# Optimization experiments

Measured on AMD Instinct MI355X. Metric: run time of the kernel, lower is better.

The kernel has to match this reference:

```python
import jax, jax.numpy as jnp
import numpy as np
import itertools

EPS = 1e-3  # BatchNorm1d eps in the original module
N_VOX = 100000


def _build_sparse_structure():
    """Build realistic clustered voxel coords, a 3x3x3 submanifold neighbor
    table (spconv rulebook equivalent), and the unique-merge mapping used by
    sum_duplicates. All index structure is constant (non-differentiable)."""
    rng = np.random.default_rng(0)
    B, Z, Y, X = 2, 40, 1600, 1408  # sparse_shape = grid_size[::-1] + [1,0,0]
    offs01 = np.array(list(itertools.product([0, 1], repeat=3)), dtype=np.int64)
    coords = []
    for b in range(B):
        base = np.stack([rng.integers(0, Z - 1, 13000),
                         rng.integers(0, Y - 1, 13000),
                         rng.integers(0, X - 1, 13000)], 1)
        exp = (base[:, None, :] + offs01[None]).reshape(-1, 3)  # clustered voxels
        coords.append(np.concatenate([np.full((len(exp), 1), b, np.int64), exp], 1))
    coords = np.unique(np.concatenate(coords, 0), axis=0)[:N_VOX]
    assert len(coords) == N_VOX
    # lexicographic unique order => encoded keys are sorted ascending
    key = ((coords[:, 0] * Z + coords[:, 1]) * Y + coords[:, 2]) * X + coords[:, 3]
    offs27 = np.array(list(itertools.product([-1, 0, 1], repeat=3)), np.int64)
    nc = coords[:, None, 1:] + offs27[None]  # [N,27,3]
    inb = (nc >= 0).all(-1) & (nc[..., 0] < Z) & (nc[..., 1] < Y) & (nc[..., 2] < X)
    nk = ((coords[:, None, 0] * Z + nc[..., 0]) * Y + nc[..., 1]) * X + nc[..., 2]
    pos = np.searchsorted(key, nk).clip(0, N_VOX - 1)
    valid = inb & (key[pos] == nk)
    nbr_idx = np.where(valid, pos, -1).astype(np.int32)  # [N,27], -1 = empty
    # second sparse tensor: half its voxels coincide, half are shifted in x
    coords2 = coords.copy()
    coords2[::2, 3] = np.minimum(coords2[::2, 3] + 1, X - 1)
    comb = np.concatenate([coords, coords2], 0)
    uniq, inv = np.unique(comb, axis=0, return_inverse=True)
    return nbr_idx, inv.astype(np.int32), int(len(uniq))


def setup_inputs() -> dict:
    nbr_idx, seg_ids, num_segments = _build_sparse_structure()
    key = jax.random.key(0)
    ks = jax.random.split(key, 6)
    C = 16
    return {
        'voxel_features': jax.random.normal(ks[0], (N_VOX, C), jnp.float32),
        'feat2': jax.random.normal(ks[1], (N_VOX, C), jnp.float32),
        'W0': jax.random.normal(ks[2], (27, C, 16), jnp.float32) * 0.1,
        'g0': jnp.ones((16,), jnp.float32),
        'b0': jnp.zeros((16,), jnp.float32),
        'W1': jax.random.normal(ks[3], (27, 16, 16), jnp.float32) * 0.1,
        'g1': jnp.ones((16,), jnp.float32),
        'b1': jnp.zeros((16,), jnp.float32),
        'Wobo': jax.random.normal(ks[4], (16, 16), jnp.float32) * 0.1,
        'bobo': jnp.zeros((16,), jnp.float32),
        'Wf': jax.random.normal(ks[5], (16, 128), jnp.float32) * 0.1,
        'bf': jnp.zeros((128,), jnp.float32),
        'nbr_idx': jnp.asarray(nbr_idx),
        'seg_ids': jnp.asarray(seg_ids),
        'num_segments': num_segments,
    }


def _subm_bn_relu(x, W, g, b, nbr_idx):
    """Submanifold 3x3x3 sparse conv (gather->GEMM) + BatchNorm1d + ReLU."""
    N = x.shape[0]
    xp = jnp.concatenate([x, jnp.zeros((1, x.shape[1]), x.dtype)], 0)  # pad row
    idx = jnp.where(nbr_idx < 0, N, nbr_idx)  # missing neighbor -> zero row
    y = jnp.einsum('nkc,kco->no', xp[idx], W)  # [N,27,Cin] x [27,Cin,Cout]
    mu = y.mean(0)
    var = y.var(0)
    return jax.nn.relu((y - mu) * jax.lax.rsqrt(var + EPS) * g + b)


def reference(voxel_features, feat2, W0, g0, b0, W1, g1, b1, Wobo, bobo, Wf, bf,
              nbr_idx, seg_ids, num_segments):
    # level-0 conv_input + conv1 (subm conv, BN, ReLU)
    h = _subm_bn_relu(voxel_features, W0, g0, b0, nbr_idx)
    h = _subm_bn_relu(h, W1, g1, b1, nbr_idx)
    # obo_* 1x1 sparse conv on the second branch (plain matmul + bias)
    t2 = feat2 @ Wobo + bobo
    # sum_duplicates: merge coincident sparse indices by summing features
    comb = jnp.concatenate([h, t2], 0)  # [2N,16]
    merged = jax.ops.segment_sum(comb, seg_ids, num_segments=num_segments)
    # final 1x1 sparse conv
    return merged @ Wf + bf  # [U,128]
```

## Files before the change

### kernel.cpp

```cpp
#include <hip/hip_runtime.h>

#define BN_EPS 1e-3f

using bfrag  = __attribute__((ext_vector_type(8))) short;
using f32x4v = __attribute__((ext_vector_type(4))) float;

__device__ __forceinline__ unsigned short f2bf(float f) {
    union { float f; unsigned u; } v; v.f = f;
    unsigned r = v.u + 0x7FFFu + ((v.u >> 16) & 1u);
    return (unsigned short)(r >> 16);
}

__global__ __launch_bounds__(256)
void prep_kernel(const float* __restrict__ vf,
                 const float* __restrict__ W0, const float* __restrict__ W1,
                 const float* __restrict__ Wf, const int* __restrict__ seg,
                 unsigned short* __restrict__ xb0,
                 unsigned short* __restrict__ Wb0, unsigned short* __restrict__ Wb1,
                 unsigned short* __restrict__ Wfb,
                 float* __restrict__ stats,
                 int* __restrict__ hidx, int* __restrict__ t2s, int N)
{
    int t = blockIdx.x * 256 + threadIdx.x;
    int TA = 2 * (N + 1);
    unsigned short tmp[8];
    if (t < TA) {
        int n = t >> 1, h = t & 1;
        if (n < N) {
            const float* yr = vf + (size_t)n * 16 + h * 8;
#pragma unroll
            for (int j = 0; j < 8; ++j) tmp[j] = f2bf(yr[j]);
        } else {
#pragma unroll
            for (int j = 0; j < 8; ++j) tmp[j] = 0;
        }
        *(int4*)(xb0 + (size_t)n * 16 + h * 8) = *(int4*)tmp;
        return;
    }
    t -= TA;
    if (t < 2 * 14 * 64) {
        int w = t >= 896;
        int l = t - w * 896;
        int s = l >> 6, lane = l & 63;
        int q = lane >> 4, n = lane & 15;
        int tap = 2 * s + (q >> 1);
        int cb  = (q & 1) * 8;
        const float* W = w ? W1 : W0;
        unsigned short* Wb = w ? Wb1 : Wb0;
#pragma unroll
        for (int j = 0; j < 8; ++j)
            tmp[j] = (tap < 27) ? f2bf(W[((size_t)(tap * 16 + cb + j)) * 16 + n]) : 0;
        *(int4*)(Wb + (size_t)l * 8) = *(int4*)tmp;
        return;
    }
    t -= 2 * 14 * 64;
    if (t < 512) {
        int ct = t >> 6, lane = t & 63;
        int q = lane >> 4, n = lane & 15;
#pragma unroll
        for (int j = 0; j < 8; ++j)
            tmp[j] = (q < 2) ? f2bf(Wf[(size_t)(q * 8 + j) * 128 + ct * 16 + n]) : 0;
        *(int4*)(Wfb + (size_t)t * 8) = *(int4*)tmp;
        return;
    }
    t -= 512;
    if (t < 64) { stats[t] = 0.f; return; }
    t -= 64;
    if (t < N) { hidx[seg[t]] = t; return; }
    t -= N;
    if (t < N) {
        int s = seg[N + t];
        if (t == 0 || seg[N + t - 1] != s) t2s[s] = t;
    }
}

__global__ __launch_bounds__(256)
void conv_mfma_kernel(const unsigned short* __restrict__ xb,
                      const unsigned short* __restrict__ Wb,
                      const int* __restrict__ nbr,
                      float* __restrict__ y,
                      float* __restrict__ partials,
                      int N)
{
    __shared__ int   sNbr[64 * 27];
    __shared__ float sred[32];
    int tid = threadIdx.x;
    if (tid < 32) sred[tid] = 0.f;

    int gb = blockIdx.x * 1728;
    int NT = N * 27;
#pragma unroll
    for (int i = 0; i < 7; ++i) {
        int t = i * 256 + tid;
        if (t < 1728) {
            int g = gb + t;
            sNbr[t] = (g < NT) ? nbr[g] : -1;
        }
    }
    __syncthreads();

    int lane = tid & 63, wib = tid >> 6;
    int q = lane >> 4, m = lane & 15;
    int c0   = (q & 1) * 8;
    int tpar = q >> 1;
    int lvox = wib * 16 + m;
    int base = blockIdx.x * 64 + wib * 16;

    int idx[14];
#pragma unroll
    for (int s = 0; s < 14; ++s) {
        int tap = 2 * s + tpar;
        int id  = (tap < 27) ? sNbr[lvox * 27 + tap] : -1;
        idx[s]  = (id >= 0) ? id : N;
    }

    f32x4v acc = {0.f, 0.f, 0.f, 0.f};
#pragma unroll
    for (int s = 0; s < 14; ++s) {
        bfrag a = *(const bfrag*)(xb + (size_t)idx[s] * 16 + c0);
        bfrag b = *(const bfrag*)(Wb + ((size_t)s * 64 + lane) * 8);
        acc = __builtin_amdgcn_mfma_f32_16x16x32_bf16(a, b, acc, 0, 0, 0);
    }

    int o = lane & 15;
#pragma unroll
    for (int i = 0; i < 4; ++i) {
        int row = base + q * 4 + i;
        if (row < N) y[(size_t)row * 16 + o] = acc[i];
    }
    float s  = acc[0] + acc[1] + acc[2] + acc[3];
    float qq = acc[0] * acc[0] + acc[1] * acc[1] + acc[2] * acc[2] + acc[3] * acc[3];
    s  += __shfl_xor(s, 16);  s  += __shfl_xor(s, 32);
    qq += __shfl_xor(qq, 16); qq += __shfl_xor(qq, 32);
    if (lane < 16) {
        atomicAdd(&sred[lane], s);
        atomicAdd(&sred[16 + lane], qq);
    }
    __syncthreads();
    if (tid < 32) partials[(size_t)blockIdx.x * 32 + tid] = sred[tid];
}

__global__ __launch_bounds__(256)
void stats_reduce_kernel(const float* __restrict__ partials,
                         float* __restrict__ stats, int nb)
{
    __shared__ float red[8][32];
    int c = threadIdx.x & 31, sl = threadIdx.x >> 5;
    float s = 0.f;
    for (int i = blockIdx.x * 8 + sl; i < nb; i += gridDim.x * 8)
        s += partials[(size_t)i * 32 + c];
    red[sl][c] = s;
    __syncthreads();
    if (threadIdx.x < 32) {
        float v = 0.f;
#pragma unroll
        for (int k = 0; k < 8; ++k) v += red[k][threadIdx.x];
        atomicAdd(&stats[threadIdx.x], v);
    }
}

__global__ __launch_bounds__(256)
void bnrelu_cvt_kernel(const float* __restrict__ y0, const float* __restrict__ stats,
                       const float* __restrict__ g, const float* __restrict__ b,
                       float invN, unsigned short* __restrict__ xb, int N)
{
    int t = blockIdx.x * 256 + threadIdx.x;
    if (t >= (N + 1) * 2) return;
    int n = t >> 1, h = t & 1;
    unsigned short tmp[8];
    if (n < N) {
        const float* yr = y0 + (size_t)n * 16 + h * 8;
#pragma unroll
        for (int j = 0; j < 8; ++j) {
            int c = h * 8 + j;
            float mu  = stats[c] * invN;
            float var = stats[16 + c] * invN - mu * mu;
            float sc  = g[c] * rsqrtf(var + BN_EPS);
            float v   = fmaxf(fmaf(yr[j], sc, b[c] - mu * sc), 0.f);
            tmp[j] = f2bf(v);
        }
    } else {
#pragma unroll
        for (int j = 0; j < 8; ++j) tmp[j] = 0;
    }
    *(int4*)(xb + (size_t)n * 16 + h * 8) = *(int4*)tmp;
}

__global__ __launch_bounds__(256)
void merge_final_kernel(const float* __restrict__ y1, const float* __restrict__ stats,
                        const float* __restrict__ g, const float* __restrict__ b,
                        float invN,
                        const float* __restrict__ feat2, const float* __restrict__ Wobo,
                        const float* __restrict__ bobo,
                        const int* __restrict__ seg,
                        const int* __restrict__ hidx, const int* __restrict__ t2s,
                        const unsigned short* __restrict__ Wfb,
                        const float* __restrict__ bf,
                        float* __restrict__ out, int N, int U)
{
    __shared__ unsigned short smA[64 * 16];
    int tid = threadIdx.x;
    int u0  = blockIdx.x * 64;

    if (tid < 128) {
        int sl = tid >> 1, half = tid & 1;
        int u  = u0 + sl;
        float m[8];
#pragma unroll
        for (int j = 0; j < 8; ++j) m[j] = 0.f;
        if (u < U) {
            int hi = hidx[u];
            if ((unsigned)hi < (unsigned)N && seg[hi] == u) {
                const float4* yr = (const float4*)(y1 + (size_t)hi * 16 + half * 8);
                float4 v0 = yr[0], v1 = yr[1];
                float mv[8];
                *(float4*)(mv + 0) = v0; *(float4*)(mv + 4) = v1;
#pragma unroll
                for (int j = 0; j < 8; ++j) {
                    int c = half * 8 + j;
                    float mu  = stats[c] * invN;
                    float var = stats[16 + c] * invN - mu * mu;
                    float sc  = g[c] * rsqrtf(var + BN_EPS);
                    m[j] = fmaxf(fmaf(mv[j], sc, b[c] - mu * sc), 0.f);
                }
            }
            int r = t2s[u];
            if ((unsigned)r < (unsigned)N && seg[N + r] == u) {
                float a2[8];
#pragma unroll
                for (int j = 0; j < 8; ++j) a2[j] = bobo[half * 8 + j];
                do {
                    const float4* fr = (const float4*)(feat2 + (size_t)r * 16);
                    float4 f0 = fr[0], f1 = fr[1], f2 = fr[2], f3 = fr[3];
                    float fv[16];
                    *(float4*)(fv + 0)  = f0; *(float4*)(fv + 4)  = f1;
                    *(float4*)(fv + 8)  = f2; *(float4*)(fv + 12) = f3;
#pragma unroll
                    for (int c = 0; c < 16; ++c) {
                        float xc = fv[c];
                        const float* wr = Wobo + c * 16 + half * 8;
#pragma unroll
                        for (int j = 0; j < 8; ++j) a2[j] = fmaf(xc, wr[j], a2[j]);
                    }
                    ++r;
                } while (r < N && seg[N + r] == u);
#pragma unroll
                for (int j = 0; j < 8; ++j) m[j] += a2[j];
            }
        }
        unsigned short tb[8];
#pragma unroll
        for (int j = 0; j < 8; ++j) tb[j] = f2bf(m[j]);
        *(int4*)(smA + (size_t)tid * 8) = *(int4*)tb;
    }
    __syncthreads();

    int lane = tid & 63, w = tid >> 6;
    int q = lane >> 4, n = lane & 15;
    bfrag a = {0, 0, 0, 0, 0, 0, 0, 0};
    if (q < 2)
        a = *(const bfrag*)(smA + ((size_t)(w * 16 + n) * 16 + q * 8));

#pragma unroll
    for (int ct = 0; ct < 8; ++ct) {
        bfrag bb = *(const bfrag*)(Wfb + ((size_t)(ct * 64 + lane)) * 8);
        f32x4v acc = {0.f, 0.f, 0.f, 0.f};
        acc = __builtin_amdgcn_mfma_f32_16x16x32_bf16(a, bb, acc, 0, 0, 0);
        int col = ct * 16 + n;
        float bv = bf[col];
#pragma unroll
        for (int i = 0; i < 4; ++i) {
            int u = u0 + w * 16 + q * 4 + i;
            if (u < U) out[(size_t)u * 128 + col] = acc[i] + bv;
        }
    }
}

extern "C" void kernel_launch(void* const* d_in, const int* in_sizes, int n_in,
                              void* d_out, int out_size, void* d_ws, size_t ws_size,
                              hipStream_t stream)
{
    const float* vf    = (const float*)d_in[0];
    const float* feat2 = (const float*)d_in[1];
    const float* W0    = (const float*)d_in[2];
    const float* g0    = (const float*)d_in[3];
    const float* b0    = (const float*)d_in[4];
    const float* W1    = (const float*)d_in[5];
    const float* g1    = (const float*)d_in[6];
    const float* b1    = (const float*)d_in[7];
    const float* Wobo  = (const float*)d_in[8];
    const float* bobo  = (const float*)d_in[9];
    const float* Wf    = (const float*)d_in[10];
    const float* bf    = (const float*)d_in[11];
    const int*   nbr   = (const int*)d_in[12];
    const int*   seg   = (const int*)d_in[13];

    int N = in_sizes[0] / 16;
    int U = out_size / 128;

    float* out = (float*)d_out;
    float* ws  = (float*)d_ws;

    int gbConv = (N + 63) / 64;

    float* y0    = ws;
    float* y1    = y0 + (size_t)N * 16;
    float* stats = y1 + (size_t)N * 16;
    float* part0 = stats + 64;
    float* part1 = part0 + (size_t)gbConv * 32;
    unsigned short* xb0 = (unsigned short*)(part1 + (size_t)gbConv * 32);
    unsigned short* xb1 = xb0 + (size_t)(N + 1) * 16;
    unsigned short* Wb0 = xb1 + (size_t)(N + 1) * 16;
    unsigned short* Wb1 = Wb0 + 14 * 64 * 8;
    unsigned short* Wfb = Wb1 + 14 * 64 * 8;
    int* hidx = (int*)(Wfb + 8 * 64 * 8);
    int* t2s  = hidx + U;

    float invN  = 1.f / (float)N;
    int thrPrep = 2 * (N + 1) + 2 * 14 * 64 + 512 + 64 + 2 * N;
    int gbPrep  = (thrPrep + 255) / 256;
    int gbCvt   = ((N + 1) * 2 + 255) / 256;

    prep_kernel<<<gbPrep, 256, 0, stream>>>(vf, W0, W1, Wf, seg, xb0, Wb0, Wb1,
                                            Wfb, stats, hidx, t2s, N);
    conv_mfma_kernel<<<gbConv, 256, 0, stream>>>(xb0, Wb0, nbr, y0, part0, N);
    stats_reduce_kernel<<<32, 256, 0, stream>>>(part0, stats, gbConv);
    bnrelu_cvt_kernel<<<gbCvt, 256, 0, stream>>>(y0, stats, g0, b0, invN, xb1, N);
    conv_mfma_kernel<<<gbConv, 256, 0, stream>>>(xb1, Wb1, nbr, y1, part1, N);
    stats_reduce_kernel<<<32, 256, 0, stream>>>(part1, stats + 32, gbConv);
    merge_final_kernel<<<(U + 63) / 64, 256, 0, stream>>>(y1, stats + 32, g1, b1, invN,
                                                          feat2, Wobo, bobo, seg,
                                                          hidx, t2s, Wfb, bf, out, N, U);
}
```

Measured before the change: 177.4 us.

## Fuse all stages into one cooperative persistent kernel with grid syncs

Replaces the seven-kernel pipeline (prep, two convs, two stat reductions, BN convert, merge/final GEMM) with a single cooperative kernel. Phases are separated by grid.sync and loop over tiles with a grid-stride pattern. BN statistics go through shared-memory accumulation and then atomics into 32 striped global slots, which replaces the separate partial-sum reduction kernels. The aim is to remove launch overhead and inter-kernel gaps. In exchange it adds grid-wide barriers, limits the grid to the resident block count, and relies on float atomics, so summation order is no longer deterministic.

```diff
diff --git a/kernel.cpp b/kernel.cpp
--- a/kernel.cpp
+++ b/kernel.cpp
@@ -1,6 +1,10 @@
 #include <hip/hip_runtime.h>
+#include <hip/hip_cooperative_groups.h>
+
+namespace cg = cooperative_groups;
 
 #define BN_EPS 1e-3f
+#define STATC  32
 
 using bfrag  = __attribute__((ext_vector_type(8))) short;
 using f32x4v = __attribute__((ext_vector_type(4))) float;
@@ -10,6 +14,293 @@
     unsigned r = v.u + 0x7FFFu + ((v.u >> 16) & 1u);
     return (unsigned short)(r >> 16);
 }
+
+
+__device__ __forceinline__ void conv_phase(
+    const unsigned short* __restrict__ xb, const unsigned short* __restrict__ Wb,
+    const int* __restrict__ nbr, float* __restrict__ y, float* __restrict__ statsC,
+    int N, int* sNbr, float* sred)
+{
+    const int tid = threadIdx.x;
+    if (tid < 32) sred[tid] = 0.f;
+    const int nTiles = (N + 63) >> 6;
+    const int NT = N * 27;
+    const int lane = tid & 63, wib = tid >> 6;
+    const int q = lane >> 4, m = lane & 15;
+    const int c0   = (q & 1) * 8;
+    const int tpar = q >> 1;
+    const int lvox = wib * 16 + m;
+
+    for (int tile = blockIdx.x; tile < nTiles; tile += gridDim.x) {
+        const int gb = tile * 1728;
+#pragma unroll
+        for (int i = 0; i < 7; ++i) {
+            int t = i * 256 + tid;
+            if (t < 1728) { int g = gb + t; sNbr[t] = (g < NT) ? nbr[g] : -1; }
+        }
+        __syncthreads();
+
+        int idx[14];
+#pragma unroll
+        for (int s = 0; s < 14; ++s) {
+            int tap = 2 * s + tpar;
+            int id  = (tap < 27) ? sNbr[lvox * 27 + tap] : -1;
+            idx[s]  = (id >= 0) ? id : N;
+        }
+
+        f32x4v acc = {0.f, 0.f, 0.f, 0.f};
+#pragma unroll
+        for (int s = 0; s < 14; ++s) {
+            bfrag a = *(const bfrag*)(xb + (size_t)idx[s] * 16 + c0);
+            bfrag b = *(const bfrag*)(Wb + ((size_t)s * 64 + lane) * 8);
+            acc = __builtin_amdgcn_mfma_f32_16x16x32_bf16(a, b, acc, 0, 0, 0);
+        }
+
+        const int base = tile * 64 + wib * 16;
+#pragma unroll
+        for (int i = 0; i < 4; ++i) {
+            int row = base + q * 4 + i;
+            if (row < N) y[(size_t)row * 16 + m] = acc[i];
+        }
+        float s  = acc[0] + acc[1] + acc[2] + acc[3];
+        float qq = acc[0]*acc[0] + acc[1]*acc[1] + acc[2]*acc[2] + acc[3]*acc[3];
+        s  += __shfl_xor(s, 16);  s  += __shfl_xor(s, 32);
+        qq += __shfl_xor(qq, 16); qq += __shfl_xor(qq, 32);
+        if (lane < 16) {
+            atomicAdd(&sred[lane], s);
+            atomicAdd(&sred[16 + lane], qq);
+        }
+        __syncthreads();
+    }
+    if (tid < 32)
+        atomicAdd(&statsC[(blockIdx.x & (STATC - 1)) * 32 + tid], sred[tid]);
+}
+
+__device__ __forceinline__ void compute_bn(
+    const float* __restrict__ statsC, const float* __restrict__ g,
+    const float* __restrict__ b, float invN, float* sSc, float* sSh, float* sred)
+{
+    const int tid = threadIdx.x;
+    __syncthreads();
+    if (tid < 32) {
+        float v = 0.f;
+#pragma unroll
+        for (int k = 0; k < STATC; ++k) v += statsC[k * 32 + tid];
+        sred[tid] = v;
+    }
+    __syncthreads();
+    if (tid < 16) {
+        float mu  = sred[tid] * invN;
+        float var = sred[16 + tid] * invN - mu * mu;
+        float sc  = g[tid] * rsqrtf(var + BN_EPS);
+        sSc[tid] = sc;
+        sSh[tid] = b[tid] - mu * sc;
+    }
+    __syncthreads();
+}
+
+__global__ __launch_bounds__(256)
+void fused_kernel(const float* __restrict__ vf, const float* __restrict__ feat2,
+                  const float* __restrict__ W0, const float* __restrict__ g0,
+                  const float* __restrict__ b0,
+                  const float* __restrict__ W1, const float* __restrict__ g1,
+                  const float* __restrict__ b1,
+                  const float* __restrict__ Wobo, const float* __restrict__ bobo,
+                  const float* __restrict__ Wf, const float* __restrict__ bfin,
+                  const int* __restrict__ nbr, const int* __restrict__ seg,
+                  float* __restrict__ y0, float* __restrict__ y1,
+                  float* __restrict__ statsA,
+                  unsigned short* __restrict__ xb0, unsigned short* __restrict__ xb1,
+                  unsigned short* __restrict__ Wb0, unsigned short* __restrict__ Wb1,
+                  unsigned short* __restrict__ Wfb,
+                  int* __restrict__ hidx, int* __restrict__ t2s,
+                  float* __restrict__ out, int N, int U)
+{
+    cg::grid_group grid = cg::this_grid();
+    __shared__ int   sNbr[64 * 27];
+    __shared__ float sred[32];
+    __shared__ float sSc[16], sSh[16];
+    __shared__ unsigned short smA[64 * 16];
+
+    const int tid = threadIdx.x;
+    const int bid = blockIdx.x;
+    const int NB  = gridDim.x;
+    const long gstride = (long)NB * 256;
+    const float invN = 1.f / (float)N;
+    float* statsB = statsA + STATC * 32;
+
+    {
+        const int TA = 2 * (N + 1);
+        const int TW = 2 * 14 * 64;
+        const int TF = 512;
+        const int TZ = 2 * STATC * 32;
+        const long T = (long)TA + TW + TF + TZ + 2L * N;
+        for (long tt = (long)bid * 256 + tid; tt < T; tt += gstride) {
+            int t = (int)tt;
+            unsigned short tmp[8];
+            if (t < TA) {
+                int n = t >> 1, h = t & 1;
+                if (n < N) {
+                    const float* yr = vf + (size_t)n * 16 + h * 8;
+#pragma unroll
+                    for (int j = 0; j < 8; ++j) tmp[j] = f2bf(yr[j]);
+                } else {
+#pragma unroll
+                    for (int j = 0; j < 8; ++j) tmp[j] = 0;
+                }
+                *(int4*)(xb0 + (size_t)n * 16 + h * 8) = *(int4*)tmp;
+            } else if ((t -= TA) < TW) {
+                int w = t >= 896;
+                int l = t - w * 896;
+                int s = l >> 6, ln = l & 63;
+                int qq = ln >> 4, n = ln & 15;
+                int tap = 2 * s + (qq >> 1);
+                int cb  = (qq & 1) * 8;
+                const float* W = w ? W1 : W0;
+                unsigned short* Wb = w ? Wb1 : Wb0;
+#pragma unroll
+                for (int j = 0; j < 8; ++j)
+                    tmp[j] = (tap < 27) ? f2bf(W[((size_t)(tap * 16 + cb + j)) * 16 + n])
+                                        : (unsigned short)0;
+                *(int4*)(Wb + (size_t)l * 8) = *(int4*)tmp;
+            } else if ((t -= TW) < TF) {
+                int ct = t >> 6, ln = t & 63;
+                int qq = ln >> 4, n = ln & 15;
+#pragma unroll
+                for (int j = 0; j < 8; ++j)
+                    tmp[j] = (qq < 2) ? f2bf(Wf[(size_t)(qq * 8 + j) * 128 + ct * 16 + n])
+                                      : (unsigned short)0;
+                *(int4*)(Wfb + (size_t)t * 8) = *(int4*)tmp;
+            } else if ((t -= TF) < TZ) {
+                statsA[t] = 0.f;
+            } else {
+                t -= TZ;
+                if (t < N) {
+                    hidx[seg[t]] = t;
+                } else {
+                    t -= N;
+                    int s = seg[N + t];
+                    if (t == 0 || seg[N + t - 1] != s) t2s[s] = t;
+                }
+            }
+        }
+    }
+    __threadfence();
+    grid.sync();
+
+    conv_phase(xb0, Wb0, nbr, y0, statsA, N, sNbr, sred);
+    __threadfence();
+    grid.sync();
+
+    compute_bn(statsA, g0, b0, invN, sSc, sSh, sred);
+    {
+        const int T2 = (N + 1) * 2;
+        for (long tt = (long)bid * 256 + tid; tt < T2; tt += gstride) {
+            int t = (int)tt;
+            int n = t >> 1, h = t & 1;
+            unsigned short tmp[8];
+            if (n < N) {
+                const float4* yr4 = (const float4*)(y0 + (size_t)n * 16 + h * 8);
+                float4 v0 = yr4[0], v1 = yr4[1];
+                float mv[8];
+                *(float4*)(mv + 0) = v0; *(float4*)(mv + 4) = v1;
+#pragma unroll
+                for (int j = 0; j < 8; ++j) {
+                    int c = h * 8 + j;
+                    tmp[j] = f2bf(fmaxf(fmaf(mv[j], sSc[c], sSh[c]), 0.f));
+                }
+            } else {
+#pragma unroll
+                for (int j = 0; j < 8; ++j) tmp[j] = 0;
+            }
+            *(int4*)(xb1 + (size_t)n * 16 + h * 8) = *(int4*)tmp;
+        }
+    }
+    __threadfence();
+    grid.sync();
+
+    conv_phase(xb1, Wb1, nbr, y1, statsB, N, sNbr, sred);
+    __threadfence();
+    grid.sync();
+
+    compute_bn(statsB, g1, b1, invN, sSc, sSh, sred);
+    {
+        const int nTileM = (U + 63) >> 6;
+        const int lane = tid & 63, w = tid >> 6;
+        const int q = lane >> 4, n16 = lane & 15;
+        for (int tile = bid; tile < nTileM; tile += NB) {
+            const int u0 = tile * 64;
+            if (tid < 128) {
+                int sl = tid >> 1, half = tid & 1;
+                int u  = u0 + sl;
+                float mm[8];
+#pragma unroll
+                for (int j = 0; j < 8; ++j) mm[j] = 0.f;
+                if (u < U) {
+                    int hi = hidx[u];
+                    if ((unsigned)hi < (unsigned)N && seg[hi] == u) {
+                        const float4* yr = (const float4*)(y1 + (size_t)hi * 16 + half * 8);
+                        float4 v0 = yr[0], v1 = yr[1];
+                        float mv[8];
+                        *(float4*)(mv + 0) = v0; *(float4*)(mv + 4) = v1;
+#pragma unroll
+                        for (int j = 0; j < 8; ++j) {
+                            int c = half * 8 + j;
+                            mm[j] = fmaxf(fmaf(mv[j], sSc[c], sSh[c]), 0.f);
+                        }
+                    }
+                    int r = t2s[u];
+                    if ((unsigned)r < (unsigned)N && seg[N + r] == u) {
+                        float a2[8];
+#pragma unroll
+                        for (int j = 0; j < 8; ++j) a2[j] = bobo[half * 8 + j];
+                        do {
+                            const float4* fr = (const float4*)(feat2 + (size_t)r * 16);
+                            float4 f0 = fr[0], f1 = fr[1], f2 = fr[2], f3 = fr[3];
+                            float fv[16];
+                            *(float4*)(fv + 0)  = f0; *(float4*)(fv + 4)  = f1;
+                            *(float4*)(fv + 8)  = f2; *(float4*)(fv + 12) = f3;
+#pragma unroll
+                            for (int c = 0; c < 16; ++c) {
+                                float xc = fv[c];
+                                const float* wr = Wobo + c * 16 + half * 8;
+#pragma unroll
+                                for (int j = 0; j < 8; ++j) a2[j] = fmaf(xc, wr[j], a2[j]);
+                            }
+                            ++r;
+                        } while (r < N && seg[N + r] == u);
+#pragma unroll
+                        for (int j = 0; j < 8; ++j) mm[j] += a2[j];
+                    }
+                }
+                unsigned short tb[8];
+#pragma unroll
+                for (int j = 0; j < 8; ++j) tb[j] = f2bf(mm[j]);
+                *(int4*)(smA + (size_t)tid * 8) = *(int4*)tb;
+            }
+            __syncthreads();
+
+            bfrag a = {0, 0, 0, 0, 0, 0, 0, 0};
+            if (q < 2)
+                a = *(const bfrag*)(smA + ((size_t)(w * 16 + n16) * 16 + q * 8));
+#pragma unroll
+            for (int ct = 0; ct < 8; ++ct) {
+                bfrag bb = *(const bfrag*)(Wfb + ((size_t)(ct * 64 + lane)) * 8);
+                f32x4v acc = {0.f, 0.f, 0.f, 0.f};
+                acc = __builtin_amdgcn_mfma_f32_16x16x32_bf16(a, bb, acc, 0, 0, 0);
+                int col = ct * 16 + n16;
+                float bv = bfin[col];
+#pragma unroll
+                for (int i = 0; i < 4; ++i) {
+                    int u = u0 + w * 16 + q * 4 + i;
+                    if (u < U) out[(size_t)u * 128 + col] = acc[i] + bv;
+                }
+            }
+            __syncthreads();
+        }
+    }
+}
+
 
 __global__ __launch_bounds__(256)
 void prep_kernel(const float* __restrict__ vf,
@@ -276,6 +567,7 @@
     }
 }
 
+
 extern "C" void kernel_launch(void* const* d_in, const int* in_sizes, int n_in,
                               void* d_out, int out_size, void* d_ws, size_t ws_size,
                               hipStream_t stream)
@@ -291,7 +583,7 @@
     const float* Wobo  = (const float*)d_in[8];
     const float* bobo  = (const float*)d_in[9];
     const float* Wf    = (const float*)d_in[10];
-    const float* bf    = (const float*)d_in[11];
+    const float* bfp   = (const float*)d_in[11];
     const int*   nbr   = (const int*)d_in[12];
     const int*   seg   = (const int*)d_in[13];
 
@@ -301,8 +593,40 @@
     float* out = (float*)d_out;
     float* ws  = (float*)d_ws;
 
+    static int  NB = 0;
+    static bool coopOK = true;
+    if (NB == 0) {
+        int mab = 0;
+        hipError_t e = hipOccupancyMaxActiveBlocksPerMultiprocessor(
+            &mab, fused_kernel, 256, 0);
+        if (e != hipSuccess || mab < 1) mab = 1;
+        NB = mab * 256;
+        if (NB > 2048) NB = 2048;
+    }
+
+    if (coopOK) {
+        float* y0     = ws;
+        float* y1     = y0 + (size_t)N * 16;
+        float* statsA = y1 + (size_t)N * 16;
+        unsigned short* xb0 = (unsigned short*)(statsA + 2 * STATC * 32);
+        unsigned short* xb1 = xb0 + (size_t)(N + 1) * 16;
+        unsigned short* Wb0 = xb1 + (size_t)(N + 1) * 16;
+        unsigned short* Wb1 = Wb0 + 14 * 64 * 8;
+        unsigned short* Wfb = Wb1 + 14 * 64 * 8;
+        int* hidx = (int*)(Wfb + 8 * 64 * 8);
+        int* t2s  = hidx + U;
+
+        void* args[] = { &vf, &feat2, &W0, &g0, &b0, &W1, &g1, &b1,
+                         &Wobo, &bobo, &Wf, &bfp, &nbr, &seg,
+                         &y0, &y1, &statsA, &xb0, &xb1, &Wb0, &Wb1, &Wfb,
+                         &hidx, &t2s, &out, &N, &U };
+        hipError_t le = hipLaunchCooperativeKernel(
+            (const void*)fused_kernel, dim3(NB), dim3(256), args, 0, stream);
+        if (le == hipSuccess) return;
+        coopOK = false;
+    }
+
     int gbConv = (N + 63) / 64;
-
     float* y0    = ws;
     float* y1    = y0 + (size_t)N * 16;
     float* stats = y1 + (size_t)N * 16;
@@ -330,5 +654,5 @@
     stats_reduce_kernel<<<32, 256, 0, stream>>>(part1, stats + 32, gbConv);
     merge_final_kernel<<<(U + 63) / 64, 256, 0, stream>>>(y1, stats + 32, g1, b1, invN,
                                                           feat2, Wobo, bobo, seg,
-                                                          hidx, t2s, Wfb, bf, out, N, U);
-}
+                                                          hidx, t2s, Wfb, bfp, out, N, U);
+}
```

New measurement: 435.4 us. 145% more time.

## Fold BN stats reduction into conv via striped atomics, drop reduce kernels

Applied to the files above, without the earlier changes.

Conv blocks now atomically add their per-channel sums into one of 32 striped slots instead of writing per-block partials. The two stats_reduce launches are removed. The BN consumer kernels sum the 32 slots once per block and precompute scale and shift in shared memory. Nontemporal loads and stores are also added to the streaming buffers (inputs, neighbor table, feat2, output). This removes two kernel launches and the partials round trip, at the cost of atomic contention and a small redundant per-block reduction.

```diff
diff --git a/kernel.cpp b/kernel.cpp
--- a/kernel.cpp
+++ b/kernel.cpp
@@ -1,6 +1,7 @@
 #include <hip/hip_runtime.h>
 
 #define BN_EPS 1e-3f
+#define STATC  32
 
 using bfrag  = __attribute__((ext_vector_type(8))) short;
 using f32x4v = __attribute__((ext_vector_type(4))) float;
@@ -27,9 +28,11 @@
     if (t < TA) {
         int n = t >> 1, h = t & 1;
         if (n < N) {
-            const float* yr = vf + (size_t)n * 16 + h * 8;
-#pragma unroll
-            for (int j = 0; j < 8; ++j) tmp[j] = f2bf(yr[j]);
+            const f32x4v* yr = (const f32x4v*)(vf + (size_t)n * 16 + h * 8);
+            f32x4v v0 = __builtin_nontemporal_load(yr);
+            f32x4v v1 = __builtin_nontemporal_load(yr + 1);
+#pragma unroll
+            for (int j = 0; j < 4; ++j) { tmp[j] = f2bf(v0[j]); tmp[4 + j] = f2bf(v1[j]); }
         } else {
 #pragma unroll
             for (int j = 0; j < 8; ++j) tmp[j] = 0;
@@ -64,8 +67,8 @@
         return;
     }
     t -= 512;
-    if (t < 64) { stats[t] = 0.f; return; }
-    t -= 64;
+    if (t < 2 * STATC * 32) { stats[t] = 0.f; return; }
+    t -= 2 * STATC * 32;
     if (t < N) { hidx[seg[t]] = t; return; }
     t -= N;
     if (t < N) {
@@ -75,12 +78,12 @@
 }
 
 __global__ __launch_bounds__(256)
-void conv_mfma_kernel(const unsigned short* __restrict__ xb,
-                      const unsigned short* __restrict__ Wb,
-                      const int* __restrict__ nbr,
-                      float* __restrict__ y,
-                      float* __restrict__ partials,
-                      int N)
+void conv_stats_kernel(const unsigned short* __restrict__ xb,
+                       const unsigned short* __restrict__ Wb,
+                       const int* __restrict__ nbr,
+                       float* __restrict__ y,
+                       float* __restrict__ statsC,
+                       int N)
 {
     __shared__ int   sNbr[64 * 27];
     __shared__ float sred[32];
@@ -94,7 +97,7 @@
         int t = i * 256 + tid;
         if (t < 1728) {
             int g = gb + t;
-            sNbr[t] = (g < NT) ? nbr[g] : -1;
+            sNbr[t] = (g < NT) ? __builtin_nontemporal_load(nbr + g) : -1;
         }
     }
     __syncthreads();
@@ -137,47 +140,47 @@
         atomicAdd(&sred[16 + lane], qq);
     }
     __syncthreads();
-    if (tid < 32) partials[(size_t)blockIdx.x * 32 + tid] = sred[tid];
+    if (tid < 32)
+        atomicAdd(&statsC[(blockIdx.x & (STATC - 1)) * 32 + tid], sred[tid]);
 }
 
 __global__ __launch_bounds__(256)
-void stats_reduce_kernel(const float* __restrict__ partials,
-                         float* __restrict__ stats, int nb)
-{
-    __shared__ float red[8][32];
-    int c = threadIdx.x & 31, sl = threadIdx.x >> 5;
-    float s = 0.f;
-    for (int i = blockIdx.x * 8 + sl; i < nb; i += gridDim.x * 8)
-        s += partials[(size_t)i * 32 + c];
-    red[sl][c] = s;
-    __syncthreads();
-    if (threadIdx.x < 32) {
-        float v = 0.f;
-#pragma unroll
-        for (int k = 0; k < 8; ++k) v += red[k][threadIdx.x];
-        atomicAdd(&stats[threadIdx.x], v);
-    }
-}
-
-__global__ __launch_bounds__(256)
-void bnrelu_cvt_kernel(const float* __restrict__ y0, const float* __restrict__ stats,
+void bnrelu_cvt_kernel(const float* __restrict__ y0, const float* __restrict__ statsC,
                        const float* __restrict__ g, const float* __restrict__ b,
                        float invN, unsigned short* __restrict__ xb, int N)
 {
-    int t = blockIdx.x * 256 + threadIdx.x;
+    __shared__ float sred[32];
+    __shared__ float sSc[16], sSh[16];
+    int tid = threadIdx.x;
+    if (tid < 32) {
+        float v = 0.f;
+#pragma unroll
+        for (int k = 0; k < STATC; ++k) v += statsC[k * 32 + tid];
+        sred[tid] = v;
+    }
+    __syncthreads();
+    if (tid < 16) {
+        float mu  = sred[tid] * invN;
+        float var = sred[16 + tid] * invN - mu * mu;
+        float sc  = g[tid] * rsqrtf(var + BN_EPS);
+        sSc[tid] = sc;
+        sSh[tid] = b[tid] - mu * sc;
+    }
+    __syncthreads();
+
+    int t = blockIdx.x * 256 + tid;
     if (t >= (N + 1) * 2) return;
     int n = t >> 1, h = t & 1;
     unsigned short tmp[8];
     if (n < N) {
-        const float* yr = y0 + (size_t)n * 16 + h * 8;
-#pragma unroll
-        for (int j = 0; j < 8; ++j) {
+        const f32x4v* yr4 = (const f32x4v*)(y0 + (size_t)n * 16 + h * 8);
+        f32x4v v0 = __builtin_nontemporal_load(yr4);
+        f32x4v v1 = __builtin_nontemporal_load(yr4 + 1);
+#pragma unroll
+        for (int j = 0; j < 4; ++j) {
             int c = h * 8 + j;
-            float mu  = stats[c] * invN;
-            float var = stats[16 + c] * invN - mu * mu;
-            float sc  = g[c] * rsqrtf(var + BN_EPS);
-            float v   = fmaxf(fmaf(yr[j], sc, b[c] - mu * sc), 0.f);
-            tmp[j] = f2bf(v);
+            tmp[j]     = f2bf(fmaxf(fmaf(v0[j], sSc[c], sSh[c]), 0.f));
+            tmp[4 + j] = f2bf(fmaxf(fmaf(v1[j], sSc[c + 4], sSh[c + 4]), 0.f));
         }
     } else {
 #pragma unroll
@@ -187,7 +190,7 @@
 }
 
 __global__ __launch_bounds__(256)
-void merge_final_kernel(const float* __restrict__ y1, const float* __restrict__ stats,
+void merge_final_kernel(const float* __restrict__ y1, const float* __restrict__ statsC,
                         const float* __restrict__ g, const float* __restrict__ b,
                         float invN,
                         const float* __restrict__ feat2, const float* __restrict__ Wobo,
@@ -199,8 +202,26 @@
                         float* __restrict__ out, int N, int U)
 {
     __shared__ unsigned short smA[64 * 16];
+    __shared__ float sred[32];
+    __shared__ float sSc[16], sSh[16];
     int tid = threadIdx.x;
     int u0  = blockIdx.x * 64;
+
+    if (tid < 32) {
+        float v = 0.f;
+#pragma unroll
+        for (int k = 0; k < STATC; ++k) v += statsC[k * 32 + tid];
+        sred[tid] = v;
+    }
+    __syncthreads();
+    if (tid < 16) {
+        float mu  = sred[tid] * invN;
+        float var = sred[16 + tid] * invN - mu * mu;
+        float sc  = g[tid] * rsqrtf(var + BN_EPS);
+        sSc[tid] = sc;
+        sSh[tid] = b[tid] - mu * sc;
+    }
+    __syncthreads();
 
     if (tid < 128) {
         int sl = tid >> 1, half = tid & 1;
@@ -218,10 +239,7 @@
 #pragma unroll
                 for (int j = 0; j < 8; ++j) {
                     int c = half * 8 + j;
-                    float mu  = stats[c] * invN;
-                    float var = stats[16 + c] * invN - mu * mu;
-                    float sc  = g[c] * rsqrtf(var + BN_EPS);
-                    m[j] = fmaxf(fmaf(mv[j], sc, b[c] - mu * sc), 0.f);
+                    m[j] = fmaxf(fmaf(mv[j], sSc[c], sSh[c]), 0.f);
                 }
             }
             int r = t2s[u];
@@ -230,11 +248,14 @@
 #pragma unroll
                 for (int j = 0; j < 8; ++j) a2[j] = bobo[half * 8 + j];
                 do {
-                    const float4* fr = (const float4*)(feat2 + (size_t)r * 16);
-                    float4 f0 = fr[0], f1 = fr[1], f2 = fr[2], f3 = fr[3];
+                    const f32x4v* fr = (const f32x4v*)(feat2 + (size_t)r * 16);
+                    f32x4v f0 = __builtin_nontemporal_load(fr);
+                    f32x4v f1 = __builtin_nontemporal_load(fr + 1);
+                    f32x4v f2 = __builtin_nontemporal_load(fr + 2);
+                    f32x4v f3 = __builtin_nontemporal_load(fr + 3);
                     float fv[16];
-                    *(float4*)(fv + 0)  = f0; *(float4*)(fv + 4)  = f1;
-                    *(float4*)(fv + 8)  = f2; *(float4*)(fv + 12) = f3;
+                    *(f32x4v*)(fv + 0)  = f0; *(f32x4v*)(fv + 4)  = f1;
+                    *(f32x4v*)(fv + 8)  = f2; *(f32x4v*)(fv + 12) = f3;
 #pragma unroll
                     for (int c = 0; c < 16; ++c) {
                         float xc = fv[c];
@@ -271,7 +292,8 @@
 #pragma unroll
         for (int i = 0; i < 4; ++i) {
             int u = u0 + w * 16 + q * 4 + i;
-            if (u < U) out[(size_t)u * 128 + col] = acc[i] + bv;
+            if (u < U)
+                __builtin_nontemporal_store(acc[i] + bv, &out[(size_t)u * 128 + col]);
         }
     }
 }
@@ -303,12 +325,11 @@
 
     int gbConv = (N + 63) / 64;
 
-    float* y0    = ws;
-    float* y1    = y0 + (size_t)N * 16;
-    float* stats = y1 + (size_t)N * 16;
-    float* part0 = stats + 64;
-    float* part1 = part0 + (size_t)gbConv * 32;
-    unsigned short* xb0 = (unsigned short*)(part1 + (size_t)gbConv * 32);
+    float* y0     = ws;
+    float* y1     = y0 + (size_t)N * 16;
+    float* statsA = y1 + (size_t)N * 16;
+    float* statsB = statsA + STATC * 32;
+    unsigned short* xb0 = (unsigned short*)(statsB + STATC * 32);
     unsigned short* xb1 = xb0 + (size_t)(N + 1) * 16;
     unsigned short* Wb0 = xb1 + (size_t)(N + 1) * 16;
     unsigned short* Wb1 = Wb0 + 14 * 64 * 8;
@@ -317,18 +338,16 @@
     int* t2s  = hidx + U;
 
     float invN  = 1.f / (float)N;
-    int thrPrep = 2 * (N + 1) + 2 * 14 * 64 + 512 + 64 + 2 * N;
+    int thrPrep = 2 * (N + 1) + 2 * 14 * 64 + 512 + 2 * STATC * 32 + 2 * N;
     int gbPrep  = (thrPrep + 255) / 256;
     int gbCvt   = ((N + 1) * 2 + 255) / 256;
 
     prep_kernel<<<gbPrep, 256, 0, stream>>>(vf, W0, W1, Wf, seg, xb0, Wb0, Wb1,
-                                            Wfb, stats, hidx, t2s, N);
-    conv_mfma_kernel<<<gbConv, 256, 0, stream>>>(xb0, Wb0, nbr, y0, part0, N);
-    stats_reduce_kernel<<<32, 256, 0, stream>>>(part0, stats, gbConv);
-    bnrelu_cvt_kernel<<<gbCvt, 256, 0, stream>>>(y0, stats, g0, b0, invN, xb1, N);
-    conv_mfma_kernel<<<gbConv, 256, 0, stream>>>(xb1, Wb1, nbr, y1, part1, N);
-    stats_reduce_kernel<<<32, 256, 0, stream>>>(part1, stats + 32, gbConv);
-    merge_final_kernel<<<(U + 63) / 64, 256, 0, stream>>>(y1, stats + 32, g1, b1, invN,
+                                            Wfb, statsA, hidx, t2s, N);
+    conv_stats_kernel<<<gbConv, 256, 0, stream>>>(xb0, Wb0, nbr, y0, statsA, N);
+    bnrelu_cvt_kernel<<<gbCvt, 256, 0, stream>>>(y0, statsA, g0, b0, invN, xb1, N);
+    conv_stats_kernel<<<gbConv, 256, 0, stream>>>(xb1, Wb1, nbr, y1, statsB, N);
+    merge_final_kernel<<<(U + 63) / 64, 256, 0, stream>>>(y1, statsB, g1, b1, invN,
                                                           feat2, Wobo, bobo, seg,
                                                           hidx, t2s, Wfb, bf, out, N, U);
 }
```

After: 177.1 us. About the same (-0.2%).
